# Performance work log

Hardware: AMD Instinct MI355X
Metric: run time of the kernel (lower is better)

## Reference

```python
import jax, jax.numpy as jnp
import numpy as np

VOCAB = 30000
FEAT = 30000
HID = 1024
EMB = 1024
B, LQ, LKV = 32, 256, 256


def setup_inputs() -> dict:
    key = jax.random.key(0)
    ks = jax.random.split(key, 8)
    captions = jax.random.randint(ks[0], (B, LKV), 0, VOCAB)
    targets_feature = jax.random.randint(ks[1], (B, LKV), 0, FEAT)
    hidden_state = jax.random.normal(ks[2], (B, LQ, HID), dtype=jnp.float32)
    feature_mask = jax.random.uniform(ks[3], (B, LQ, LKV), dtype=jnp.float32)
    # embeddings initialized uniform(-0.1, 0.1) per init_weights
    Wa = jax.random.uniform(ks[4], (VOCAB, HID), minval=-0.1, maxval=0.1, dtype=jnp.float32)
    Wc = jax.random.uniform(ks[5], (FEAT, HID), minval=-0.1, maxval=0.1, dtype=jnp.float32)
    r = np.sqrt(6.0) / np.sqrt(2 * HID + EMB)
    fc_w = jax.random.uniform(ks[6], (EMB, 2 * HID), minval=-r, maxval=r, dtype=jnp.float32)
    fc_b = jnp.zeros((EMB,), dtype=jnp.float32)
    return {"captions": captions, "hidden_state": hidden_state,
            "targets_feature": targets_feature, "feature_mask": feature_mask,
            "Wa": Wa, "Wc": Wc, "fc_w": fc_w, "fc_b": fc_b}


def reference(captions, hidden_state, targets_feature, feature_mask, Wa, Wc, fc_w, fc_b):
    ea = Wa[captions]           # [B, LKV, H]
    ec = Wc[targets_feature]    # [B, LKV, H]
    # u = hidden_state @ embedding_a^T : [B, LQ, LKV]
    u = jnp.einsum('bqh,bkh->bqk', hidden_state, ea)
    mask = jnp.clip(feature_mask, 0.0, 1.0)
    delta = jnp.exp(u) * mask
    p = delta / (jnp.sum(delta, axis=2, keepdims=True) + 1e-10)  # masked softmax-like weights
    # weighted value sum without materializing [B,LQ,LKV,H] broadcasts
    o = jnp.einsum('bqk,bkh->bqh', p, ec)
    o = jnp.concatenate([hidden_state, o], axis=2)               # [B, LQ, 2H]
    o = o @ fc_w.T + fc_b                                        # [B, LQ, EMB]
    o = o + 1e-10
    norm = jnp.sqrt(jnp.sum(o * o, axis=-1, keepdims=True)) + 1e-8
    return o / norm
```

## Files before the change

### kernel.cpp

```cpp
#include <hip/hip_runtime.h>
#include <hip/hip_bf16.h>

typedef __attribute__((ext_vector_type(8))) short short8;
typedef __attribute__((ext_vector_type(4))) float f32x4;
using bf16 = __hip_bfloat16;


__device__ __forceinline__ void glds16(const void* g, void* lds) {
  __builtin_amdgcn_global_load_lds(
      (const __attribute__((address_space(1))) void*)g,
      (__attribute__((address_space(3))) void*)lds, 16, 0, 0);
}

__global__ __launch_bounds__(256) void k1_prep(
    const int* __restrict__ captions, const float* __restrict__ Wa,
    const float* __restrict__ H, const float* __restrict__ fcw,
    const int* __restrict__ targets, const float* __restrict__ Wc,
    bf16* __restrict__ EA, bf16* __restrict__ X, bf16* __restrict__ FW,
    bf16* __restrict__ ECT) {
  __shared__ float T[64][67];
  int task = blockIdx.x;
  int tid = threadIdx.x;
  if (task < 17408) {
    const float* src;
    bf16* dst;
    int n;
    if (task < 8192) {
      src = Wa + (size_t)captions[task] * 1024;
      dst = EA + (size_t)task * 1024;
      n = 1024;
    } else if (task < 16384) {
      int t = task - 8192;
      src = H + (size_t)t * 1024;
      dst = X + (size_t)t * 2048;
      n = 1024;
    } else {
      int t = task - 16384;
      src = fcw + (size_t)t * 2048;
      dst = FW + (size_t)t * 2048;
      n = 2048;
    }
    for (int c = tid * 4; c < n; c += 1024) {
      float4 v = *(const float4*)(src + c);
      __hip_bfloat162 p0, p1;
      p0.x = __float2bfloat16(v.x); p0.y = __float2bfloat16(v.y);
      p1.x = __float2bfloat16(v.z); p1.y = __float2bfloat16(v.w);
      *(__hip_bfloat162*)(dst + c) = p0;
      *(__hip_bfloat162*)(dst + c + 2) = p1;
    }
    return;
  }
  int bid = task - 17408;
  int b = bid >> 6;
  int kt = (bid >> 4) & 3;
  int ht = bid & 15;
#pragma unroll
  for (int p = 0; p < 4; ++p) {
    int k = p * 16 + (tid >> 4);
    int idx = targets[b * 256 + kt * 64 + k];
    const float* s = Wc + (size_t)idx * 1024 + ht * 64 + (tid & 15) * 4;
    float4 v = *(const float4*)s;
    int c = (tid & 15) * 4;
    T[k][c] = v.x; T[k][c + 1] = v.y; T[k][c + 2] = v.z; T[k][c + 3] = v.w;
  }
  __syncthreads();
#pragma unroll
  for (int p = 0; p < 8; ++p) {
    int h = p * 8 + (tid >> 5);
    int k = (tid & 31) * 2;
    __hip_bfloat162 o;
    o.x = __float2bfloat16(T[k][h]);
    o.y = __float2bfloat16(T[k + 1][h]);
    *(__hip_bfloat162*)(ECT + ((size_t)b * 1024 + ht * 64 + h) * 256 + kt * 64 + k) = o;
  }
}

__global__ __launch_bounds__(256, 1) void k23_scores_pv(
    bf16* __restrict__ X, const bf16* __restrict__ EA,
    const bf16* __restrict__ ECT, const float* __restrict__ mask) {
  __shared__ __align__(16) char smem[16 * 1024 + 512 + 128 * 1024];
  bf16* p_lds = (bf16*)smem;
  float* red  = (float*)(smem + 16 * 1024);
  bf16* big   = (bf16*)(smem + 16 * 1024 + 512);

  int p = blockIdx.x;
  int wg = (p & 7) * 32 + (p >> 3);
  int b = wg >> 3;
  int mb = wg & 7;
  int tid = threadIdx.x, w = tid >> 6, l = tid & 63;

  const bf16* Ag = X + ((size_t)b * 256 + mb * 32) * 2048;
  const bf16* Bg = EA + (size_t)b * 256 * 1024;
  bf16* As = big;
  bf16* Bs = big + 32 * 64;

  f32x4 sacc[2][4];
  f32x4 zero = {0.f, 0.f, 0.f, 0.f};
#pragma unroll
  for (int m2 = 0; m2 < 2; ++m2)
#pragma unroll
    for (int n = 0; n < 4; ++n) sacc[m2][n] = zero;

  for (int kt = 0; kt < 16; ++kt) {
    {
      int row = tid >> 3, ss = (tid & 7) ^ (row & 7);
      glds16(Ag + (size_t)row * 2048 + kt * 64 + ss * 8,
             As + (size_t)w * 64 * 8);
    }
#pragma unroll
    for (int i = 0; i < 8; ++i) {
      int c = i * 256 + tid;
      int row = c >> 3, ss = (c & 7) ^ (row & 7);
      glds16(Bg + (size_t)row * 1024 + kt * 64 + ss * 8,
             Bs + (size_t)(i * 256 + w * 64) * 8);
    }
    __syncthreads();
#pragma unroll
    for (int kk = 0; kk < 2; ++kk) {
      short8 a2[2];
#pragma unroll
      for (int m2 = 0; m2 < 2; ++m2) {
        int ar = m2 * 16 + (l & 15);
        int sl = kk * 4 + (l >> 4);
        a2[m2] = *(const short8*)(As + ar * 64 + ((sl ^ (ar & 7)) * 8));
      }
      __builtin_amdgcn_s_setprio(1);
#pragma unroll
      for (int n = 0; n < 4; ++n) {
        int rb = w * 64 + n * 16 + (l & 15);
        int sl = kk * 4 + (l >> 4);
        short8 bfr = *(const short8*)(Bs + rb * 64 + ((sl ^ (rb & 7)) * 8));
#pragma unroll
        for (int m2 = 0; m2 < 2; ++m2)
          sacc[m2][n] = __builtin_amdgcn_mfma_f32_16x16x32_bf16(
              a2[m2], bfr, sacc[m2][n], 0, 0, 0);
      }
      __builtin_amdgcn_s_setprio(0);
    }
    __syncthreads();
  }

  const float* mrow = mask + ((size_t)b * 256 + mb * 32) * 256;
  float s[2][4] = {{0.f, 0.f, 0.f, 0.f}, {0.f, 0.f, 0.f, 0.f}};
#pragma unroll
  for (int m2 = 0; m2 < 2; ++m2)
#pragma unroll
    for (int n = 0; n < 4; ++n)
#pragma unroll
      for (int i = 0; i < 4; ++i) {
        int r = m2 * 16 + ((l >> 4) << 2) + i;
        int c = w * 64 + n * 16 + (l & 15);
        float mv = mrow[r * 256 + c];
        mv = fminf(fmaxf(mv, 0.f), 1.f);
        float ev = expf(sacc[m2][n][i]) * mv;
        sacc[m2][n][i] = ev;
        s[m2][i] += ev;
      }
#pragma unroll
  for (int msk = 1; msk < 16; msk <<= 1)
#pragma unroll
    for (int m2 = 0; m2 < 2; ++m2)
#pragma unroll
      for (int i = 0; i < 4; ++i) s[m2][i] += __shfl_xor(s[m2][i], msk, 64);
  if ((l & 15) == 0) {
#pragma unroll
    for (int m2 = 0; m2 < 2; ++m2)
#pragma unroll
      for (int i = 0; i < 4; ++i)
        red[w * 32 + m2 * 16 + ((l >> 4) << 2) + i] = s[m2][i];
  }
  __syncthreads();
  float inv[2][4];
#pragma unroll
  for (int m2 = 0; m2 < 2; ++m2)
#pragma unroll
    for (int i = 0; i < 4; ++i) {
      int r = m2 * 16 + ((l >> 4) << 2) + i;
      float tot = red[r] + red[32 + r] + red[64 + r] + red[96 + r];
      inv[m2][i] = 1.f / (tot + 1e-10f);
    }
#pragma unroll
  for (int m2 = 0; m2 < 2; ++m2)
#pragma unroll
    for (int n = 0; n < 4; ++n)
#pragma unroll
      for (int i = 0; i < 4; ++i) {
        int r = m2 * 16 + ((l >> 4) << 2) + i;
        int c = w * 64 + n * 16 + (l & 15);
        float pv = sacc[m2][n][i] * inv[m2][i];
        p_lds[r * 256 + (((c >> 3) ^ (r & 7)) << 3) + (c & 7)] =
            __float2bfloat16(pv);
      }
  __syncthreads();

  bf16* XO = X + ((size_t)b * 256 + mb * 32) * 2048 + 1024;
  for (int np = 0; np < 2; ++np) {
    f32x4 acc[2][8];
#pragma unroll
    for (int m2 = 0; m2 < 2; ++m2)
#pragma unroll
      for (int n = 0; n < 8; ++n) acc[m2][n] = zero;

#pragma unroll
    for (int it = 0; it < 16; ++it) {
      int g = it * 64 + l;
      int row = g >> 3, ss = (g & 7) ^ (row & 7);
      glds16(ECT + ((size_t)b * 1024 + np * 512 + w * 128 + row) * 256 + ss * 8,
             big + (size_t)(0 * 4 + w) * 8192 + (size_t)it * 512);
    }
    __syncthreads();
    for (int kt = 0; kt < 4; ++kt) {
      int cur = kt & 1;
      if (kt < 3) {
#pragma unroll
        for (int it = 0; it < 16; ++it) {
          int g = it * 64 + l;
          int row = g >> 3, ss = (g & 7) ^ (row & 7);
          glds16(ECT + ((size_t)b * 1024 + np * 512 + w * 128 + row) * 256 +
                     (kt + 1) * 64 + ss * 8,
                 big + (size_t)((cur ^ 1) * 4 + w) * 8192 + (size_t)it * 512);
        }
      }
      const bf16* Bw = big + (size_t)(cur * 4 + w) * 8192;
#pragma unroll
      for (int kk = 0; kk < 2; ++kk) {
        short8 a2[2];
#pragma unroll
        for (int m2 = 0; m2 < 2; ++m2) {
          int ar = m2 * 16 + (l & 15);
          int sl = kt * 8 + kk * 4 + (l >> 4);
          a2[m2] = *(const short8*)(p_lds + ar * 256 + ((sl ^ (ar & 7)) * 8));
        }
        __builtin_amdgcn_s_setprio(1);
#pragma unroll
        for (int n = 0; n < 8; ++n) {
          int rb = n * 16 + (l & 15);
          int sl = kk * 4 + (l >> 4);
          short8 bfr = *(const short8*)(Bw + rb * 64 + ((sl ^ (rb & 7)) * 8));
#pragma unroll
          for (int m2 = 0; m2 < 2; ++m2)
            acc[m2][n] = __builtin_amdgcn_mfma_f32_16x16x32_bf16(
                a2[m2], bfr, acc[m2][n], 0, 0, 0);
        }
        __builtin_amdgcn_s_setprio(0);
      }
      __syncthreads();
    }
#pragma unroll
    for (int m2 = 0; m2 < 2; ++m2)
#pragma unroll
      for (int n = 0; n < 8; ++n) {
        int rl = m2 * 16 + ((l >> 4) << 2);
        int col = np * 512 + w * 128 + n * 16 + (l & 15);
#pragma unroll
        for (int i = 0; i < 4; ++i)
          XO[(size_t)(rl + i) * 2048 + col] = __float2bfloat16(acc[m2][n][i]);
      }
  }
}

#define K4A (256 * 64)
#define K4B (128 * 64)

__device__ __forceinline__ void k4_stage(const bf16* __restrict__ Ag,
                                         const bf16* __restrict__ Bg, int kt,
                                         bf16* As, bf16* Bs, int tid, int w) {
#pragma unroll
  for (int i = 0; i < 4; ++i) {
    int c = i * 512 + tid;
    int row = c >> 3, ss = (c & 7) ^ (row & 7);
    glds16(Ag + (size_t)row * 2048 + kt * 64 + ss * 8,
           As + (size_t)(i * 512 + w * 64) * 8);
  }
#pragma unroll
  for (int i = 0; i < 2; ++i) {
    int c = i * 512 + tid;
    int row = c >> 3, ss = (c & 7) ^ (row & 7);
    glds16(Bg + (size_t)row * 2048 + kt * 64 + ss * 8,
           Bs + (size_t)(i * 512 + w * 64) * 8);
  }
}

__device__ __forceinline__ void k4_tile(const bf16* As, const bf16* Bs,
                                        int wr, int wc, int l,
                                        f32x4 (&acc)[4][4]) {
  short8 a[2][4], b[2][4];
#pragma unroll
  for (int kk = 0; kk < 2; ++kk)
#pragma unroll
    for (int n = 0; n < 4; ++n) {
      int row = wc * 64 + n * 16 + (l & 15);
      int slot = kk * 4 + (l >> 4);
      b[kk][n] = *(const short8*)(Bs + row * 64 + ((slot ^ (row & 7)) * 8));
    }
#pragma unroll
  for (int kk = 0; kk < 2; ++kk)
#pragma unroll
    for (int m = 0; m < 4; ++m) {
      int row = wr * 64 + m * 16 + (l & 15);
      int slot = kk * 4 + (l >> 4);
      a[kk][m] = *(const short8*)(As + row * 64 + ((slot ^ (row & 7)) * 8));
    }
  __builtin_amdgcn_s_setprio(1);
#pragma unroll
  for (int kk = 0; kk < 2; ++kk)
#pragma unroll
    for (int m = 0; m < 4; ++m)
#pragma unroll
      for (int n = 0; n < 4; ++n)
        acc[m][n] = __builtin_amdgcn_mfma_f32_16x16x32_bf16(
            a[kk][m], b[kk][n], acc[m][n], 0, 0, 0);
  __builtin_amdgcn_s_setprio(0);
}

__global__ __launch_bounds__(512, 1) void k4_fc(
    const bf16* __restrict__ X, const bf16* __restrict__ FW,
    const float* __restrict__ fcb, float* __restrict__ out) {
  __shared__ __align__(16) bf16 As[2][K4A];
  __shared__ __align__(16) bf16 Bs[2][K4B];
  int p = blockIdx.x;
  int wg = (p & 7) * 32 + (p >> 3);
  int mb = wg >> 3;
  int nb = wg & 7;
  int tid = threadIdx.x, w = tid >> 6, l = tid & 63;
  int wr = w >> 1, wc = w & 1;
  f32x4 acc[4][4];
  f32x4 zero = {0.f, 0.f, 0.f, 0.f};
#pragma unroll
  for (int m = 0; m < 4; ++m)
#pragma unroll
    for (int n = 0; n < 4; ++n) acc[m][n] = zero;

  const bf16* Ag = X + (size_t)mb * 256 * 2048;
  const bf16* Bg = FW + (size_t)nb * 128 * 2048;

  k4_stage(Ag, Bg, 0, As[0], Bs[0], tid, w);
  __syncthreads();
  for (int t = 0; t < 32; ++t) {
    int cur = t & 1;
    if (t < 31)
      k4_stage(Ag, Bg, t + 1, As[cur ^ 1], Bs[cur ^ 1], tid, w);
    k4_tile(As[cur], Bs[cur], wr, wc, l, acc);
    __syncthreads();
  }

  float bias[4];
#pragma unroll
  for (int n = 0; n < 4; ++n)
    bias[n] = fcb[nb * 128 + wc * 64 + n * 16 + (l & 15)];
#pragma unroll
  for (int m = 0; m < 4; ++m) {
    int rbase = mb * 256 + wr * 64 + m * 16 + ((l >> 4) << 2);
#pragma unroll
    for (int n = 0; n < 4; ++n) {
      int col = nb * 128 + wc * 64 + n * 16 + (l & 15);
#pragma unroll
      for (int i = 0; i < 4; ++i)
        out[(size_t)(rbase + i) * 1024 + col] = acc[m][n][i] + bias[n] + 1e-10f;
    }
  }
}

__global__ __launch_bounds__(256) void k5_norm(float* __restrict__ y) {
  __shared__ float red[4];
  int row = blockIdx.x;
  float* p = y + (size_t)row * 1024;
  int tid = threadIdx.x;
  float4 v = *(const float4*)(p + tid * 4);
  float ss = v.x * v.x + v.y * v.y + v.z * v.z + v.w * v.w;
#pragma unroll
  for (int m = 1; m < 64; m <<= 1) ss += __shfl_xor(ss, m, 64);
  if ((tid & 63) == 0) red[tid >> 6] = ss;
  __syncthreads();
  float tot = red[0] + red[1] + red[2] + red[3];
  float inv = 1.f / (sqrtf(tot) + 1e-8f);
  float4 o;
  o.x = v.x * inv; o.y = v.y * inv; o.z = v.z * inv; o.w = v.w * inv;
  *(float4*)(p + tid * 4) = o;
}

extern "C" void kernel_launch(void* const* d_in, const int* in_sizes, int n_in,
                              void* d_out, int out_size, void* d_ws, size_t ws_size,
                              hipStream_t stream) {
  const int* captions = (const int*)d_in[0];
  const float* H = (const float*)d_in[1];
  const int* targets = (const int*)d_in[2];
  const float* mask = (const float*)d_in[3];
  const float* Wa = (const float*)d_in[4];
  const float* Wc = (const float*)d_in[5];
  const float* fcw = (const float*)d_in[6];
  const float* fcb = (const float*)d_in[7];
  float* out = (float*)d_out;

  char* ws = (char*)d_ws;
  bf16* EA = (bf16*)(ws);
  bf16* ECT = (bf16*)(ws + (16u << 20));
  bf16* X = (bf16*)(ws + (36u << 20));
  bf16* FW = (bf16*)(ws + (68u << 20));

  k1_prep<<<19456, 256, 0, stream>>>(captions, Wa, H, fcw, targets, Wc,
                                     EA, X, FW, ECT);
  k23_scores_pv<<<256, 256, 0, stream>>>(X, EA, ECT, mask);
  k4_fc<<<256, 512, 0, stream>>>(X, FW, fcb, out);
  k5_norm<<<8192, 256, 0, stream>>>(out);
}
```

Measured before the change: 118.1 us.

## Fuse Wa embedding gather into scores kernel with double-buffered register prefetch

Removes the separate EA gather/convert pass from the prep kernel. The scores kernel now gathers Wa rows directly via caption indices held in LDS, converting fp32 to bf16 in registers and double-buffering the A/B tiles so the next k-tile's loads overlap the current MFMAs. The PV stage is flattened into a single 8-step loop with the first ECT tile prefetched before the softmax, so loads continue across the np boundary. This saves writing and rereading the bf16 EA buffer, at the cost of each of the 8 row-blocks per batch re-reading fp32 Wa rows (redundant global traffic) and higher register pressure.

```diff
diff --git a/kernel.cpp b/kernel.cpp
--- a/kernel.cpp
+++ b/kernel.cpp
@@ -13,29 +13,22 @@
 }
 
 __global__ __launch_bounds__(256) void k1_prep(
-    const int* __restrict__ captions, const float* __restrict__ Wa,
     const float* __restrict__ H, const float* __restrict__ fcw,
     const int* __restrict__ targets, const float* __restrict__ Wc,
-    bf16* __restrict__ EA, bf16* __restrict__ X, bf16* __restrict__ FW,
-    bf16* __restrict__ ECT) {
+    bf16* __restrict__ X, bf16* __restrict__ FW, bf16* __restrict__ ECT) {
   __shared__ float T[64][67];
   int task = blockIdx.x;
   int tid = threadIdx.x;
-  if (task < 17408) {
+  if (task < 9216) {
     const float* src;
     bf16* dst;
     int n;
     if (task < 8192) {
-      src = Wa + (size_t)captions[task] * 1024;
-      dst = EA + (size_t)task * 1024;
-      n = 1024;
-    } else if (task < 16384) {
-      int t = task - 8192;
-      src = H + (size_t)t * 1024;
-      dst = X + (size_t)t * 2048;
+      src = H + (size_t)task * 1024;
+      dst = X + (size_t)task * 2048;
       n = 1024;
     } else {
-      int t = task - 16384;
+      int t = task - 8192;
       src = fcw + (size_t)t * 2048;
       dst = FW + (size_t)t * 2048;
       n = 2048;
@@ -50,7 +43,7 @@
     }
     return;
   }
-  int bid = task - 17408;
+  int bid = task - 9216;
   int b = bid >> 6;
   int kt = (bid >> 4) & 3;
   int ht = bid & 15;
@@ -76,12 +69,14 @@
 }
 
 __global__ __launch_bounds__(256, 1) void k23_scores_pv(
-    bf16* __restrict__ X, const bf16* __restrict__ EA,
-    const bf16* __restrict__ ECT, const float* __restrict__ mask) {
-  __shared__ __align__(16) char smem[16 * 1024 + 512 + 128 * 1024];
+    bf16* __restrict__ X, const float* __restrict__ Wa,
+    const int* __restrict__ captions, const bf16* __restrict__ ECT,
+    const float* __restrict__ mask) {
+  __shared__ __align__(16) char smem[16 * 1024 + 512 + 1024 + 128 * 1024];
   bf16* p_lds = (bf16*)smem;
   float* red  = (float*)(smem + 16 * 1024);
-  bf16* big   = (bf16*)(smem + 16 * 1024 + 512);
+  int* idx_l  = (int*)(smem + 16 * 1024 + 512);
+  bf16* big   = (bf16*)(smem + 16 * 1024 + 512 + 1024);
 
   int p = blockIdx.x;
   int wg = (p & 7) * 32 + (p >> 3);
@@ -90,9 +85,8 @@
   int tid = threadIdx.x, w = tid >> 6, l = tid & 63;
 
   const bf16* Ag = X + ((size_t)b * 256 + mb * 32) * 2048;
-  const bf16* Bg = EA + (size_t)b * 256 * 1024;
-  bf16* As = big;
-  bf16* Bs = big + 32 * 64;
+  bf16* bufA[2] = {big, big + 18432};
+  bf16* bufB[2] = {big + 2048, big + 18432 + 2048};
 
   f32x4 sacc[2][4];
   f32x4 zero = {0.f, 0.f, 0.f, 0.f};
@@ -101,20 +95,50 @@
 #pragma unroll
     for (int n = 0; n < 4; ++n) sacc[m2][n] = zero;
 
+  idx_l[tid] = captions[b * 256 + tid];
+  {
+    int row = tid >> 3, ssA = (tid & 7) ^ (row & 7);
+    glds16(Ag + (size_t)row * 2048 + ssA * 8, bufA[0] + (size_t)w * 64 * 8);
+  }
+  __syncthreads();
+  {
+    float4 bv[8][2];
+#pragma unroll
+    for (int i = 0; i < 8; ++i) {
+      int row = i * 32 + w * 8 + (l >> 3);
+      int ss = (l & 7) ^ (row & 7);
+      const float* src = Wa + (size_t)idx_l[row] * 1024 + ss * 8;
+      bv[i][0] = *(const float4*)(src);
+      bv[i][1] = *(const float4*)(src + 4);
+    }
+#pragma unroll
+    for (int i = 0; i < 8; ++i) {
+      union { short8 s; __hip_bfloat16 h[8]; } u;
+      u.h[0] = __float2bfloat16(bv[i][0].x); u.h[1] = __float2bfloat16(bv[i][0].y);
+      u.h[2] = __float2bfloat16(bv[i][0].z); u.h[3] = __float2bfloat16(bv[i][0].w);
+      u.h[4] = __float2bfloat16(bv[i][1].x); u.h[5] = __float2bfloat16(bv[i][1].y);
+      u.h[6] = __float2bfloat16(bv[i][1].z); u.h[7] = __float2bfloat16(bv[i][1].w);
+      *(short8*)(bufB[0] + (size_t)(i * 256 + w * 64) * 8 + l * 8) = u.s;
+    }
+  }
+  __syncthreads();
+
   for (int kt = 0; kt < 16; ++kt) {
-    {
-      int row = tid >> 3, ss = (tid & 7) ^ (row & 7);
-      glds16(Ag + (size_t)row * 2048 + kt * 64 + ss * 8,
-             As + (size_t)w * 64 * 8);
-    }
-#pragma unroll
-    for (int i = 0; i < 8; ++i) {
-      int c = i * 256 + tid;
-      int row = c >> 3, ss = (c & 7) ^ (row & 7);
-      glds16(Bg + (size_t)row * 1024 + kt * 64 + ss * 8,
-             Bs + (size_t)(i * 256 + w * 64) * 8);
-    }
-    __syncthreads();
+    int cur = kt & 1;
+    float4 bv[8][2];
+    if (kt < 15) {
+#pragma unroll
+      for (int i = 0; i < 8; ++i) {
+        int row = i * 32 + w * 8 + (l >> 3);
+        int ss = (l & 7) ^ (row & 7);
+        const float* src = Wa + (size_t)idx_l[row] * 1024 + (kt + 1) * 64 + ss * 8;
+        bv[i][0] = *(const float4*)(src);
+        bv[i][1] = *(const float4*)(src + 4);
+      }
+      int row = tid >> 3, ssA = (tid & 7) ^ (row & 7);
+      glds16(Ag + (size_t)row * 2048 + (kt + 1) * 64 + ssA * 8,
+             bufA[cur ^ 1] + (size_t)w * 64 * 8);
+    }
 #pragma unroll
     for (int kk = 0; kk < 2; ++kk) {
       short8 a2[2];
@@ -122,14 +146,14 @@
       for (int m2 = 0; m2 < 2; ++m2) {
         int ar = m2 * 16 + (l & 15);
         int sl = kk * 4 + (l >> 4);
-        a2[m2] = *(const short8*)(As + ar * 64 + ((sl ^ (ar & 7)) * 8));
+        a2[m2] = *(const short8*)(bufA[cur] + ar * 64 + ((sl ^ (ar & 7)) * 8));
       }
       __builtin_amdgcn_s_setprio(1);
 #pragma unroll
       for (int n = 0; n < 4; ++n) {
         int rb = w * 64 + n * 16 + (l & 15);
         int sl = kk * 4 + (l >> 4);
-        short8 bfr = *(const short8*)(Bs + rb * 64 + ((sl ^ (rb & 7)) * 8));
+        short8 bfr = *(const short8*)(bufB[cur] + rb * 64 + ((sl ^ (rb & 7)) * 8));
 #pragma unroll
         for (int m2 = 0; m2 < 2; ++m2)
           sacc[m2][n] = __builtin_amdgcn_mfma_f32_16x16x32_bf16(
@@ -137,7 +161,26 @@
       }
       __builtin_amdgcn_s_setprio(0);
     }
+    if (kt < 15) {
+#pragma unroll
+      for (int i = 0; i < 8; ++i) {
+        union { short8 s; __hip_bfloat16 h[8]; } u;
+        u.h[0] = __float2bfloat16(bv[i][0].x); u.h[1] = __float2bfloat16(bv[i][0].y);
+        u.h[2] = __float2bfloat16(bv[i][0].z); u.h[3] = __float2bfloat16(bv[i][0].w);
+        u.h[4] = __float2bfloat16(bv[i][1].x); u.h[5] = __float2bfloat16(bv[i][1].y);
+        u.h[6] = __float2bfloat16(bv[i][1].z); u.h[7] = __float2bfloat16(bv[i][1].w);
+        *(short8*)(bufB[cur ^ 1] + (size_t)(i * 256 + w * 64) * 8 + l * 8) = u.s;
+      }
+    }
     __syncthreads();
+  }
+
+#pragma unroll
+  for (int it = 0; it < 16; ++it) {
+    int g = it * 64 + l;
+    int row = g >> 3, ss = (g & 7) ^ (row & 7);
+    glds16(ECT + ((size_t)b * 1024 + w * 128 + row) * 256 + ss * 8,
+           big + (size_t)w * 8192 + (size_t)it * 512);
   }
 
   const float* mrow = mask + ((size_t)b * 256 + mb * 32) * 256;
@@ -194,68 +237,64 @@
   __syncthreads();
 
   bf16* XO = X + ((size_t)b * 256 + mb * 32) * 2048 + 1024;
-  for (int np = 0; np < 2; ++np) {
-    f32x4 acc[2][8];
-#pragma unroll
-    for (int m2 = 0; m2 < 2; ++m2)
-#pragma unroll
-      for (int n = 0; n < 8; ++n) acc[m2][n] = zero;
-
-#pragma unroll
-    for (int it = 0; it < 16; ++it) {
-      int g = it * 64 + l;
-      int row = g >> 3, ss = (g & 7) ^ (row & 7);
-      glds16(ECT + ((size_t)b * 1024 + np * 512 + w * 128 + row) * 256 + ss * 8,
-             big + (size_t)(0 * 4 + w) * 8192 + (size_t)it * 512);
+  f32x4 acc[2][8];
+#pragma unroll
+  for (int m2 = 0; m2 < 2; ++m2)
+#pragma unroll
+    for (int n = 0; n < 8; ++n) acc[m2][n] = zero;
+
+  for (int idx = 0; idx < 8; ++idx) {
+    int cur = idx & 1;
+    int kt = idx & 3;
+    if (idx < 7) {
+      int jnp = (idx + 1) >> 2, jkt = (idx + 1) & 3;
+#pragma unroll
+      for (int it = 0; it < 16; ++it) {
+        int g = it * 64 + l;
+        int row = g >> 3, ss = (g & 7) ^ (row & 7);
+        glds16(ECT + ((size_t)b * 1024 + jnp * 512 + w * 128 + row) * 256 +
+                   jkt * 64 + ss * 8,
+               big + (size_t)((cur ^ 1) * 4 + w) * 8192 + (size_t)it * 512);
+      }
+    }
+    const bf16* Bw = big + (size_t)(cur * 4 + w) * 8192;
+#pragma unroll
+    for (int kk = 0; kk < 2; ++kk) {
+      short8 a2[2];
+#pragma unroll
+      for (int m2 = 0; m2 < 2; ++m2) {
+        int ar = m2 * 16 + (l & 15);
+        int sl = kt * 8 + kk * 4 + (l >> 4);
+        a2[m2] = *(const short8*)(p_lds + ar * 256 + ((sl ^ (ar & 7)) * 8));
+      }
+      __builtin_amdgcn_s_setprio(1);
+#pragma unroll
+      for (int n = 0; n < 8; ++n) {
+        int rb = n * 16 + (l & 15);
+        int sl = kk * 4 + (l >> 4);
+        short8 bfr = *(const short8*)(Bw + rb * 64 + ((sl ^ (rb & 7)) * 8));
+#pragma unroll
+        for (int m2 = 0; m2 < 2; ++m2)
+          acc[m2][n] = __builtin_amdgcn_mfma_f32_16x16x32_bf16(
+              a2[m2], bfr, acc[m2][n], 0, 0, 0);
+      }
+      __builtin_amdgcn_s_setprio(0);
+    }
+    if (idx == 3 || idx == 7) {
+      int np = idx >> 2;
+#pragma unroll
+      for (int m2 = 0; m2 < 2; ++m2)
+#pragma unroll
+        for (int n = 0; n < 8; ++n) {
+          int rl = m2 * 16 + ((l >> 4) << 2);
+          int col = np * 512 + w * 128 + n * 16 + (l & 15);
+#pragma unroll
+          for (int i = 0; i < 4; ++i)
+            XO[(size_t)(rl + i) * 2048 + col] = __float2bfloat16(acc[m2][n][i]);
+          acc[m2][n] = zero;
+        }
     }
     __syncthreads();
-    for (int kt = 0; kt < 4; ++kt) {
-      int cur = kt & 1;
-      if (kt < 3) {
-#pragma unroll
-        for (int it = 0; it < 16; ++it) {
-          int g = it * 64 + l;
-          int row = g >> 3, ss = (g & 7) ^ (row & 7);
-          glds16(ECT + ((size_t)b * 1024 + np * 512 + w * 128 + row) * 256 +
-                     (kt + 1) * 64 + ss * 8,
-                 big + (size_t)((cur ^ 1) * 4 + w) * 8192 + (size_t)it * 512);
-        }
-      }
-      const bf16* Bw = big + (size_t)(cur * 4 + w) * 8192;
-#pragma unroll
-      for (int kk = 0; kk < 2; ++kk) {
-        short8 a2[2];
-#pragma unroll
-        for (int m2 = 0; m2 < 2; ++m2) {
-          int ar = m2 * 16 + (l & 15);
-          int sl = kt * 8 + kk * 4 + (l >> 4);
-          a2[m2] = *(const short8*)(p_lds + ar * 256 + ((sl ^ (ar & 7)) * 8));
-        }
-        __builtin_amdgcn_s_setprio(1);
-#pragma unroll
-        for (int n = 0; n < 8; ++n) {
-          int rb = n * 16 + (l & 15);
-          int sl = kk * 4 + (l >> 4);
-          short8 bfr = *(const short8*)(Bw + rb * 64 + ((sl ^ (rb & 7)) * 8));
-#pragma unroll
-          for (int m2 = 0; m2 < 2; ++m2)
-            acc[m2][n] = __builtin_amdgcn_mfma_f32_16x16x32_bf16(
-                a2[m2], bfr, acc[m2][n], 0, 0, 0);
-        }
-        __builtin_amdgcn_s_setprio(0);
-      }
-      __syncthreads();
-    }
-#pragma unroll
-    for (int m2 = 0; m2 < 2; ++m2)
-#pragma unroll
-      for (int n = 0; n < 8; ++n) {
-        int rl = m2 * 16 + ((l >> 4) << 2);
-        int col = np * 512 + w * 128 + n * 16 + (l & 15);
-#pragma unroll
-        for (int i = 0; i < 4; ++i)
-          XO[(size_t)(rl + i) * 2048 + col] = __float2bfloat16(acc[m2][n][i]);
-      }
   }
 }
 
@@ -393,14 +432,12 @@
   float* out = (float*)d_out;
 
   char* ws = (char*)d_ws;
-  bf16* EA = (bf16*)(ws);
   bf16* ECT = (bf16*)(ws + (16u << 20));
   bf16* X = (bf16*)(ws + (36u << 20));
   bf16* FW = (bf16*)(ws + (68u << 20));
 
-  k1_prep<<<19456, 256, 0, stream>>>(captions, Wa, H, fcw, targets, Wc,
-                                     EA, X, FW, ECT);
-  k23_scores_pv<<<256, 256, 0, stream>>>(X, EA, ECT, mask);
+  k1_prep<<<11264, 256, 0, stream>>>(H, fcw, targets, Wc, X, FW, ECT);
+  k23_scores_pv<<<256, 256, 0, stream>>>(X, Wa, captions, ECT, mask);
   k4_fc<<<256, 512, 0, stream>>>(X, FW, fcb, out);
   k5_norm<<<8192, 256, 0, stream>>>(out);
 }
```

Measured after the change: 129.2 us. 9.4% more time.

## Triple-buffer FC GEMM LDS tiles with explicit vmcnt waits and raw barriers

Applied to the files above, without the earlier changes.

The final FC GEMM kernel moves from a double-buffered LDS pipeline with __syncthreads to a three-stage ring buffer. Loads are issued two K-tiles ahead, and partial s_waitcnt vmcnt(12) waits plus raw s_barrier calls let the next tile's global-to-LDS loads stay in flight while MFMAs run. The goal is to hide global load latency better. In exchange it uses more LDS (three stages, about 144KB) and depends on hand-placed waitcnt and scheduling barriers being exactly right.

```diff
diff --git a/kernel.cpp b/kernel.cpp
--- a/kernel.cpp
+++ b/kernel.cpp
@@ -5,11 +5,21 @@
 typedef __attribute__((ext_vector_type(4))) float f32x4;
 using bf16 = __hip_bfloat16;
 
+
+#define VMCNT(n) asm volatile("s_waitcnt vmcnt(" #n ")" ::: "memory")
+#define LGK0     asm volatile("s_waitcnt lgkmcnt(0)" ::: "memory")
+#define SBAR     __builtin_amdgcn_sched_barrier(0)
 
 __device__ __forceinline__ void glds16(const void* g, void* lds) {
   __builtin_amdgcn_global_load_lds(
       (const __attribute__((address_space(1))) void*)g,
       (__attribute__((address_space(3))) void*)lds, 16, 0, 0);
+}
+
+__device__ __forceinline__ void barrier_raw() {
+  asm volatile("" ::: "memory");
+  __builtin_amdgcn_s_barrier();
+  asm volatile("" ::: "memory");
 }
 
 __global__ __launch_bounds__(256) void k1_prep(
@@ -259,31 +269,31 @@
   }
 }
 
-#define K4A (256 * 64)
-#define K4B (128 * 64)
+#define K4E (256 * 64 + 128 * 64)
 
 __device__ __forceinline__ void k4_stage(const bf16* __restrict__ Ag,
                                          const bf16* __restrict__ Bg, int kt,
-                                         bf16* As, bf16* Bs, int tid, int w) {
+                                         bf16* Lb, int tid, int w) {
 #pragma unroll
   for (int i = 0; i < 4; ++i) {
     int c = i * 512 + tid;
     int row = c >> 3, ss = (c & 7) ^ (row & 7);
     glds16(Ag + (size_t)row * 2048 + kt * 64 + ss * 8,
-           As + (size_t)(i * 512 + w * 64) * 8);
+           Lb + (size_t)(i * 512 + w * 64) * 8);
   }
 #pragma unroll
   for (int i = 0; i < 2; ++i) {
     int c = i * 512 + tid;
     int row = c >> 3, ss = (c & 7) ^ (row & 7);
     glds16(Bg + (size_t)row * 2048 + kt * 64 + ss * 8,
-           Bs + (size_t)(i * 512 + w * 64) * 8);
-  }
-}
-
-__device__ __forceinline__ void k4_tile(const bf16* As, const bf16* Bs,
-                                        int wr, int wc, int l,
+           Lb + (size_t)(256 * 64 + (i * 512 + w * 64) * 8));
+  }
+}
+
+__device__ __forceinline__ void k4_tile(const bf16* Lb, int wr, int wc, int l,
                                         f32x4 (&acc)[4][4]) {
+  const bf16* As = Lb;
+  const bf16* Bs = Lb + 256 * 64;
   short8 a[2][4], b[2][4];
 #pragma unroll
   for (int kk = 0; kk < 2; ++kk)
@@ -316,8 +326,7 @@
 __global__ __launch_bounds__(512, 1) void k4_fc(
     const bf16* __restrict__ X, const bf16* __restrict__ FW,
     const float* __restrict__ fcb, float* __restrict__ out) {
-  __shared__ __align__(16) bf16 As[2][K4A];
-  __shared__ __align__(16) bf16 Bs[2][K4B];
+  __shared__ __align__(16) bf16 L[3][K4E];
   int p = blockIdx.x;
   int wg = (p & 7) * 32 + (p >> 3);
   int mb = wg >> 3;
@@ -334,15 +343,31 @@
   const bf16* Ag = X + (size_t)mb * 256 * 2048;
   const bf16* Bg = FW + (size_t)nb * 128 * 2048;
 
-  k4_stage(Ag, Bg, 0, As[0], Bs[0], tid, w);
-  __syncthreads();
-  for (int t = 0; t < 32; ++t) {
-    int cur = t & 1;
-    if (t < 31)
-      k4_stage(Ag, Bg, t + 1, As[cur ^ 1], Bs[cur ^ 1], tid, w);
-    k4_tile(As[cur], Bs[cur], wr, wc, l, acc);
-    __syncthreads();
-  }
+  k4_stage(Ag, Bg, 0, L[0], tid, w);
+  k4_stage(Ag, Bg, 1, L[1], tid, w);
+
+#define K4_BODY(T, C, S)                                   \
+  k4_stage(Ag, Bg, (T) + 2, L[S], tid, w);                 \
+  VMCNT(12); SBAR;                                         \
+  barrier_raw(); SBAR;                                     \
+  k4_tile(L[C], wr, wc, l, acc);                           \
+  LGK0; SBAR;                                              \
+  barrier_raw();
+
+  for (int tt = 0; tt < 30; tt += 3) {
+    K4_BODY(tt + 0, 0, 2)
+    K4_BODY(tt + 1, 1, 0)
+    K4_BODY(tt + 2, 2, 1)
+  }
+#undef K4_BODY
+  VMCNT(6); SBAR;
+  barrier_raw(); SBAR;
+  k4_tile(L[0], wr, wc, l, acc);
+  LGK0; SBAR;
+  barrier_raw();
+  VMCNT(0); SBAR;
+  barrier_raw(); SBAR;
+  k4_tile(L[1], wr, wc, l, acc);
 
   float bias[4];
 #pragma unroll
```

Measured after the change: 109.7 us. 7.1% less time.
